# Performance work log

Hardware: AMD Instinct MI355X
Metric: run time of the kernel (lower is better)

## Reference

```python
import jax, jax.numpy as jnp
import numpy as np

# dims: B batch, T seq, DM d_model, H kv heads, D head dim
B, T, DM = 4, 2048, 768
H, D = 4, 64          # n_kv_heads, d_head = d_model // n_heads = 768 // 12
DIM = H * D           # 256


def setup_inputs() -> dict:
    key = jax.random.key(0)
    kx, kq, kk, kv, ko, kg = jax.random.split(key, 6)
    s = 0.02  # init scale for weights
    return {
        "x": jax.random.normal(kx, (B, T, DM), jnp.float32),
        "Wq": jax.random.normal(kq, (DM, DIM), jnp.float32) * s,
        "Wk": jax.random.normal(kk, (DM, DIM), jnp.float32) * s,
        "Wv": jax.random.normal(kv, (DM, DIM), jnp.float32) * s,
        "Wo": jax.random.normal(ko, (DIM, DM), jnp.float32) * s,
        "Wg": jax.random.normal(kg, (DM, DM), jnp.float32) * s,
    }


def _feature_map(x):
    # F.elu(x) + 1.0  (strictly positive features)
    return jax.nn.elu(x) + 1.0


def reference(x, Wq, Wk, Wv, Wo, Wg):
    Bx, Tx, _ = x.shape
    q = _feature_map((x @ Wq).reshape(Bx, Tx, H, D))
    k = _feature_map((x @ Wk).reshape(Bx, Tx, H, D))
    v = (x @ Wv).reshape(Bx, Tx, H, D)

    # time-major for scan: [T, B, H, D]
    qT = q.transpose(1, 0, 2, 3)
    kT = k.transpose(1, 0, 2, 3)
    vT = v.transpose(1, 0, 2, 3)

    S0 = jnp.zeros((Bx, H, D, D), x.dtype)  # running sum of k v^T
    z0 = jnp.zeros((Bx, H, D), x.dtype)     # running sum of k

    def step(carry, inp):
        S, z = carry
        qi, ki, vi = inp  # each [B, H, D]
        S = S + ki[..., :, None] * vi[..., None, :]   # outer product update
        z = z + ki
        num = jnp.einsum('bhd,bhde->bhe', qi, S)
        den = jnp.maximum(jnp.sum(qi * z, axis=-1), 1e-6)  # clamp(min=1e-6)
        return (S, z), num / den[..., None]

    (_, _), outT = jax.lax.scan(step, (S0, z0), (qT, kT, vT))

    out = outT.transpose(1, 0, 2, 3).reshape(Bx, Tx, DIM)  # [B, T, H*D]
    gate = jax.nn.sigmoid(x @ Wg)
    return (out @ Wo) * gate
```

## Files before the change

### kernel.cpp

```cpp
#include <hip/hip_runtime.h>
#include <math.h>

typedef __attribute__((ext_vector_type(8))) short bf16x8;
typedef __attribute__((ext_vector_type(4))) float f32x4;

namespace {
constexpr int Bb  = 4;
constexpr int Tt  = 2048;
constexpr int DM  = 768;
constexpr int Hh  = 4;
constexpr int Dd  = 64;
constexpr int DIM = 256;
constexpr int BT  = Bb * Tt;
constexpr int CH  = 64;
constexpr int NC  = Tt / CH;
constexpr int NQKVG = 1536;
constexpr int MT  = BT / 128;
}

__device__ __forceinline__ float elu1(float x) { return x > 0.f ? x + 1.f : expf(x); }

__device__ __forceinline__ unsigned short f2bf(float f) {
  unsigned int x = __float_as_uint(f);
  unsigned int r = (x + 0x7fffu + ((x >> 16) & 1u)) >> 16;
  return (unsigned short)r;
}
__device__ __forceinline__ float bf2f(unsigned short u) {
  return __uint_as_float((unsigned int)u << 16);
}

__device__ __forceinline__ void gload16(const void* g, void* l) {
  __builtin_amdgcn_global_load_lds(
      (const __attribute__((address_space(1))) void*)g,
      (__attribute__((address_space(3))) void*)l, 16, 0, 0);
}

struct Stage32 {
  const short* a[2];
  const short* b[2];
  int seg;
  __device__ __forceinline__ void init(const short* Ag, size_t lda,
                                       const short* Bg, size_t ldb, int w, int l) {
    const int c16 = (l & 3) ^ ((l >> 3) & 3);
    seg = w * 2;
#pragma unroll
    for (int j = 0; j < 2; ++j) {
      int row = (seg + j) * 16 + (l >> 2);
      a[j] = Ag + (size_t)row * lda + c16 * 8;
      b[j] = Bg + (size_t)row * ldb + c16 * 8;
    }
  }
  __device__ __forceinline__ void issue(int k0, short* as, short* bs) const {
#pragma unroll
    for (int j = 0; j < 2; ++j) {
      gload16(a[j] + k0, (char*)as + (seg + j) * 1024);
      gload16(b[j] + k0, (char*)bs + (seg + j) * 1024);
    }
  }
};

__device__ __forceinline__ void xcd_tile(int bid, int& mt, int& nt) {
  int xcd = bid & 7;
  int idx = bid >> 3;
  mt = xcd * 8 + (idx & 7);
  nt = idx >> 3;
}

__device__ __forceinline__ void read_frags(const short* as, const short* bs,
                                           bf16x8 (&af)[4], bf16x8 (&bf)[4],
                                           int wr, int wc, int lr, int lg) {
#pragma unroll
  for (int mi = 0; mi < 4; ++mi) {
    int r = wr * 64 + mi * 16 + lr;
    af[mi] = *(const bf16x8*)&as[r * 32 + (lg ^ ((r >> 1) & 3)) * 8];
  }
#pragma unroll
  for (int ni = 0; ni < 4; ++ni) {
    int r = wc * 64 + ni * 16 + lr;
    bf[ni] = *(const bf16x8*)&bs[r * 32 + (lg ^ ((r >> 1) & 3)) * 8];
  }
}

template <int NT>
__device__ __forceinline__ void kloop3p(const Stage32& st,
                                        short* A0, short* A1, short* A2,
                                        short* B0, short* B1, short* B2,
                                        f32x4 (&acc)[4][4], int wr, int wc,
                                        int lr, int lg) {
  st.issue(0, A0, B0);
  st.issue(32, A1, B1);
  asm volatile("s_waitcnt vmcnt(4)" ::: "memory");
  __builtin_amdgcn_s_barrier();
  bf16x8 af[4], bf[4];
  read_frags(A0, B0, af, bf, wr, wc, lr, lg);
  asm volatile("s_waitcnt lgkmcnt(0)" ::: "memory");
  __builtin_amdgcn_sched_barrier(0);
#pragma unroll
  for (int t = 0; t < NT; ++t) {
    if (t + 2 < NT) {
      short* an = (((t + 2) % 3) == 0) ? A0 : (((t + 2) % 3) == 1) ? A1 : A2;
      short* bn = (((t + 2) % 3) == 0) ? B0 : (((t + 2) % 3) == 1) ? B1 : B2;
      st.issue((t + 2) * 32, an, bn);
    }
    __builtin_amdgcn_s_setprio(1);
#pragma unroll
    for (int mi = 0; mi < 4; ++mi)
#pragma unroll
      for (int ni = 0; ni < 4; ++ni)
        acc[mi][ni] = __builtin_amdgcn_mfma_f32_16x16x32_bf16(
            af[mi], bf[ni], acc[mi][ni], 0, 0, 0);
    __builtin_amdgcn_s_setprio(0);
    if (t + 1 < NT) {
      if (t + 2 < NT)
        asm volatile("s_waitcnt vmcnt(4)" ::: "memory");
      else
        asm volatile("s_waitcnt vmcnt(0)" ::: "memory");
      __builtin_amdgcn_s_barrier();
      short* as = (((t + 1) % 3) == 0) ? A0 : (((t + 1) % 3) == 1) ? A1 : A2;
      short* bs = (((t + 1) % 3) == 0) ? B0 : (((t + 1) % 3) == 1) ? B1 : B2;
      read_frags(as, bs, af, bf, wr, wc, lr, lg);
      asm volatile("s_waitcnt lgkmcnt(0)" ::: "memory");
      __builtin_amdgcn_sched_barrier(0);
    }
  }
}

__global__ __launch_bounds__(256) void k_prep(
    const float* __restrict__ x, const float* __restrict__ Wq,
    const float* __restrict__ Wk, const float* __restrict__ Wv,
    const float* __restrict__ Wg, const float* __restrict__ Wo,
    unsigned short* __restrict__ xb, unsigned short* __restrict__ WT,
    unsigned short* __restrict__ WoT) {
  int bid = blockIdx.x;
  if (bid < 3072) {
    int i = bid * 256 + threadIdx.x;
    const float4* p = (const float4*)(x + (size_t)i * 8);
    float4 a = p[0], b = p[1];
    union { unsigned short u[8]; uint4 v; } r;
    r.u[0] = f2bf(a.x); r.u[1] = f2bf(a.y); r.u[2] = f2bf(a.z); r.u[3] = f2bf(a.w);
    r.u[4] = f2bf(b.x); r.u[5] = f2bf(b.y); r.u[6] = f2bf(b.z); r.u[7] = f2bf(b.w);
    *(uint4*)(xb + (size_t)i * 8) = r.v;
    return;
  }
  __shared__ float t[32][33];
  int idx = bid - 3072;
  const float* src;
  unsigned short* out;
  int K, N, n_off, ldo;
  if (idx < 576) {
    int z = idx / 192;
    idx %= 192;
    src = (z == 0) ? Wq : (z == 1) ? Wk : Wv;
    out = WT; K = 768; N = 256; n_off = z * 256; ldo = 768;
  } else if (idx < 1152) {
    idx -= 576;
    src = Wg; out = WT; K = 768; N = 768; n_off = 768; ldo = 768;
  } else {
    idx -= 1152;
    src = Wo; out = WoT; K = 256; N = 768; n_off = 0; ldo = 256;
  }
  int kt = idx % (K / 32), nt = idx / (K / 32);
  int k0 = kt * 32, n0 = nt * 32;
  const int tx = threadIdx.x & 31, ty = threadIdx.x >> 5;
  for (int i = ty; i < 32; i += 8)
    t[i][tx] = src[(size_t)(k0 + i) * N + n0 + tx];
  __syncthreads();
  for (int i = ty; i < 32; i += 8)
    out[(size_t)(n_off + n0 + i) * ldo + k0 + tx] = f2bf(t[tx][i]);
}

__global__ __launch_bounds__(256, 3) void k_gemm1(
    const unsigned short* __restrict__ xb, const unsigned short* __restrict__ WT,
    unsigned short* __restrict__ Q, unsigned short* __restrict__ K,
    unsigned short* __restrict__ V, unsigned short* __restrict__ G) {
  __shared__ __align__(16) char smem[49152];
  short* A0 = (short*)smem;
  short* A1 = (short*)(smem + 8192);
  short* A2 = (short*)(smem + 16384);
  short* B0 = (short*)(smem + 24576);
  short* B1 = (short*)(smem + 32768);
  short* B2 = (short*)(smem + 40960);
  const int tid = threadIdx.x;
  const int w = tid >> 6, l = tid & 63;
  const int lr = l & 15, lg = l >> 4;
  const int wr = w >> 1, wc = w & 1;
  int mt, nt;
  xcd_tile(blockIdx.x, mt, nt);
  const int m0 = mt * 128, n0 = nt * 128;

  Stage32 st;
  st.init((const short*)xb + (size_t)m0 * DM, DM,
          (const short*)WT + (size_t)n0 * DM, DM, w, l);

  f32x4 acc[4][4];
#pragma unroll
  for (int i = 0; i < 4; ++i)
#pragma unroll
    for (int j = 0; j < 4; ++j) acc[i][j] = (f32x4){0.f, 0.f, 0.f, 0.f};

  kloop3p<DM / 32>(st, A0, A1, A2, B0, B1, B2, acc, wr, wc, lr, lg);
  __syncthreads();

  const int ttype = (n0 < 512) ? 0 : (n0 < 768) ? 1 : 2;
  unsigned short* Cs = (unsigned short*)smem;
#pragma unroll
  for (int mi = 0; mi < 4; ++mi)
#pragma unroll
    for (int ni = 0; ni < 4; ++ni)
#pragma unroll
      for (int r = 0; r < 4; ++r) {
        float v = acc[mi][ni][r];
        if (ttype == 0) v = elu1(v);
        else if (ttype == 2) v = 1.f / (1.f + expf(-v));
        Cs[(wr * 64 + mi * 16 + lg * 4 + r) * 128 + wc * 64 + ni * 16 + lr] =
            f2bf(v);
      }
  __syncthreads();
  unsigned short* dst;
  int ldd, cb;
  if (n0 < 256)      { dst = Q; ldd = DIM; cb = n0; }
  else if (n0 < 512) { dst = K; ldd = DIM; cb = n0 - 256; }
  else if (n0 < 768) { dst = V; ldd = DIM; cb = n0 - 512; }
  else               { dst = G; ldd = DM;  cb = n0 - 768; }
  const uint4* Cv = (const uint4*)Cs;
#pragma unroll
  for (int i = 0; i < 8; ++i) {
    int idx = tid + i * 256;
    int urow = idx >> 4, uc = idx & 15;
    *(uint4*)(dst + (size_t)(m0 + urow) * ldd + cb + uc * 8) = Cv[idx];
  }
}

__global__ __launch_bounds__(256) void k_chunksum(
    const unsigned short* __restrict__ K, const unsigned short* __restrict__ V,
    unsigned short* __restrict__ Sc, float* __restrict__ zc) {
  __shared__ __align__(16) char smem[16384];
  short* Kt = (short*)smem;
  short* Vt = (short*)(smem + 8192);
  const int c = blockIdx.x, h = blockIdx.y, b = blockIdx.z;
  const int tid = threadIdx.x;
  const int w = tid >> 6, l = tid & 63;
  const int lr = l & 15, lg = l >> 4;
  const size_t rowbase = ((size_t)(b * Tt + c * CH)) * DIM + h * Dd;

#pragma unroll
  for (int it = 0; it < 4; ++it) {
    int idx = tid + it * 256;
    int t = idx >> 4, d4 = idx & 15;
    short4 k4 = *(const short4*)((const short*)K + rowbase + (size_t)t * DIM + d4 * 4);
    short4 v4 = *(const short4*)((const short*)V + rowbase + (size_t)t * DIM + d4 * 4);
    const short* kk = (const short*)&k4;
    const short* vv = (const short*)&v4;
#pragma unroll
    for (int j = 0; j < 4; ++j) {
      int e = d4 * 4 + j;
      int sl = ((t >> 3) ^ (e & 7)) * 16 + (t & 7) * 2;
      *(short*)((char*)Kt + e * 128 + sl) = kk[j];
      *(short*)((char*)Vt + e * 128 + sl) = vv[j];
    }
  }
  __syncthreads();

  if (tid < Dd) {
    float s = 0.f;
    for (int t = 0; t < CH; ++t) {
      unsigned short u = *(const unsigned short*)(
          (char*)Kt + tid * 128 + (((t >> 3) ^ (tid & 7)) * 16) + (t & 7) * 2);
      s += bf2f(u);
    }
    zc[((size_t)(b * Hh + h) * NC + c) * Dd + tid] = s;
  }

  f32x4 a[4];
#pragma unroll
  for (int nf = 0; nf < 4; ++nf) a[nf] = (f32x4){0.f, 0.f, 0.f, 0.f};
  const int rd = w * 16 + lr;
#pragma unroll
  for (int ks = 0; ks < 2; ++ks) {
    bf16x8 af = *(const bf16x8*)((char*)Kt + rd * 128 +
                                 (((ks * 4 + lg) ^ (rd & 7)) * 16));
#pragma unroll
    for (int nf = 0; nf < 4; ++nf) {
      int re = nf * 16 + lr;
      bf16x8 bf = *(const bf16x8*)((char*)Vt + re * 128 +
                                   (((ks * 4 + lg) ^ (re & 7)) * 16));
      a[nf] = __builtin_amdgcn_mfma_f32_16x16x32_bf16(af, bf, a[nf], 0, 0, 0);
    }
  }
  __syncthreads();

  unsigned short* Cb = (unsigned short*)smem;
#pragma unroll
  for (int nf = 0; nf < 4; ++nf)
#pragma unroll
    for (int r = 0; r < 4; ++r)
      Cb[(w * 16 + lg * 4 + r) * 64 + nf * 16 + lr] = f2bf(a[nf][r]);
  __syncthreads();
  const size_t base = ((size_t)(b * Hh + h) * NC + c) * (Dd * Dd);
  const uint4* Cv = (const uint4*)Cb;
#pragma unroll
  for (int it = 0; it < 2; ++it) {
    int idx = tid + it * 256;
    *(uint4*)&Sc[base + (size_t)idx * 8] = Cv[idx];
  }
}

__global__ __launch_bounds__(256) void k_scan(unsigned short* __restrict__ Sc,
                                              float* __restrict__ zc) {
  const int bh = blockIdx.x;
  const int o = blockIdx.y * 256 + threadIdx.x;
  const size_t base = (size_t)bh * NC * (Dd * Dd) + o;
  float run = 0.f;
#pragma unroll
  for (int c = 0; c < NC; ++c) {
    size_t off = base + (size_t)c * (Dd * Dd);
    float cur = bf2f(Sc[off]);
    Sc[off] = f2bf(run);
    run += cur;
  }
  if (blockIdx.y == 0 && threadIdx.x < Dd) {
    float rz = 0.f;
    for (int c = 0; c < NC; ++c) {
      size_t oz = ((size_t)bh * NC + c) * Dd + threadIdx.x;
      float cur = zc[oz];
      zc[oz] = rz;
      rz += cur;
    }
  }
}

__global__ __launch_bounds__(256) void k_out(
    const unsigned short* __restrict__ Q, const unsigned short* __restrict__ K,
    const unsigned short* __restrict__ V, const unsigned short* __restrict__ Sc,
    const float* __restrict__ zc, unsigned short* __restrict__ O) {
  __shared__ __align__(16) char smem[41216];
  short* Qs = (short*)smem;
  short* Ks = (short*)(smem + 8192);
  short* Vt = (short*)(smem + 16384);
  short* St = (short*)(smem + 24576);
  short* Ps = (short*)(smem + 32768);
  float* zs = (float*)(smem + 40960);
  const int c = blockIdx.x, h = blockIdx.y, b = blockIdx.z;
  const int tid = threadIdx.x;
  const int w = tid >> 6, l = tid & 63;
  const int lr = l & 15, lg = l >> 4;
  const size_t rowbase = ((size_t)(b * Tt + c * CH)) * DIM + h * Dd;

  {
    const int c16 = (l & 7) ^ ((l >> 3) & 7);
#pragma unroll
    for (int i = 0; i < 2; ++i) {
      int row = i * 32 + w * 8 + (l >> 3);
      gload16((const short*)Q + rowbase + (size_t)row * DIM + c16 * 8,
              (char*)Qs + (i * 32 + w * 8) * 128);
      gload16((const short*)K + rowbase + (size_t)row * DIM + c16 * 8,
              (char*)Ks + (i * 32 + w * 8) * 128);
    }
  }
  const size_t sbase = ((size_t)(b * Hh + h) * NC + c) * (Dd * Dd);
  if (tid < Dd) zs[tid] = zc[((size_t)(b * Hh + h) * NC + c) * Dd + tid];
#pragma unroll
  for (int it = 0; it < 4; ++it) {
    int idx = tid + it * 256;
    int t = idx >> 4, d4 = idx & 15;
    short4 v4 = *(const short4*)((const short*)V + rowbase + (size_t)t * DIM + d4 * 4);
    const short* vv = (const short*)&v4;
#pragma unroll
    for (int j = 0; j < 4; ++j) {
      int e = d4 * 4 + j;
      *(short*)((char*)Vt + e * 128 + (((t >> 3) ^ (e & 7)) * 16) + (t & 7) * 2) = vv[j];
    }
    short4 s4 = *(const short4*)((const short*)Sc + sbase + (size_t)t * 64 + d4 * 4);
    const short* sv = (const short*)&s4;
#pragma unroll
    for (int j = 0; j < 4; ++j) {
      int e = d4 * 4 + j;
      *(short*)((char*)St + e * 128 + (((t >> 3) ^ (e & 7)) * 16) + (t & 7) * 2) =
          sv[j];
    }
  }
  __syncthreads();

  f32x4 a0[4];
#pragma unroll
  for (int nf = 0; nf < 4; ++nf) a0[nf] = (f32x4){0.f, 0.f, 0.f, 0.f};
  const int rq = w * 16 + lr;
#pragma unroll
  for (int ks = 0; ks < 2; ++ks) {
    bf16x8 af = *(const bf16x8*)((char*)Qs + rq * 128 +
                                 (((ks * 4 + lg) ^ (rq & 7)) * 16));
#pragma unroll
    for (int nf = 0; nf < 4; ++nf) {
      int rk = nf * 16 + lr;
      bf16x8 bf = *(const bf16x8*)((char*)Ks + rk * 128 +
                                   (((ks * 4 + lg) ^ (rk & 7)) * 16));
      a0[nf] = __builtin_amdgcn_mfma_f32_16x16x32_bf16(af, bf, a0[nf], 0, 0, 0);
    }
  }

  float part[4] = {0.f, 0.f, 0.f, 0.f};
#pragma unroll
  for (int nf = 0; nf < 4; ++nf) {
    int col = nf * 16 + lr;
#pragma unroll
    for (int r = 0; r < 4; ++r) {
      int row = w * 16 + lg * 4 + r;
      float av = (col <= row) ? a0[nf][r] : 0.f;
      part[r] += av;
      *(short*)((char*)Ps + row * 128 +
                ((((nf * 2) + (lr >> 3)) ^ (row & 7)) * 16) + (lr & 7) * 2) =
          (short)f2bf(av);
    }
  }
#pragma unroll
  for (int r = 0; r < 4; ++r) {
    int row = w * 16 + lg * 4 + r;
#pragma unroll
    for (int j = 0; j < 4; ++j) {
      int d = lr + j * 16;
      unsigned short qu = *(const unsigned short*)(
          (char*)Qs + row * 128 + (((d >> 3) ^ (row & 7)) * 16) + (d & 7) * 2);
      part[r] += bf2f(qu) * zs[d];
    }
  }
  float inv[4];
#pragma unroll
  for (int r = 0; r < 4; ++r) {
    float s = part[r];
    s += __shfl_xor(s, 1);
    s += __shfl_xor(s, 2);
    s += __shfl_xor(s, 4);
    s += __shfl_xor(s, 8);
    inv[r] = 1.f / fmaxf(s, 1e-6f);
  }
  __syncthreads();

  f32x4 a1[4];
#pragma unroll
  for (int nf = 0; nf < 4; ++nf) a1[nf] = (f32x4){0.f, 0.f, 0.f, 0.f};
#pragma unroll
  for (int ks = 0; ks < 4; ++ks) {
    const char* abase = (ks < 2) ? (const char*)Ps : (const char*)Qs;
    const char* bbase = (ks < 2) ? (const char*)Vt : (const char*)St;
    int kslot = (ks & 1) * 4 + lg;
    bf16x8 af = *(const bf16x8*)(abase + rq * 128 + ((kslot ^ (rq & 7)) * 16));
#pragma unroll
    for (int nf = 0; nf < 4; ++nf) {
      int re = nf * 16 + lr;
      bf16x8 bf = *(const bf16x8*)(bbase + re * 128 + ((kslot ^ (re & 7)) * 16));
      a1[nf] = __builtin_amdgcn_mfma_f32_16x16x32_bf16(af, bf, a1[nf], 0, 0, 0);
    }
  }
  __syncthreads();

#pragma unroll
  for (int nf = 0; nf < 4; ++nf)
#pragma unroll
    for (int r = 0; r < 4; ++r) {
      int row = w * 16 + lg * 4 + r;
      Ps[row * 64 + nf * 16 + lr] = (short)f2bf(a1[nf][r] * inv[r]);
    }
  __syncthreads();
  const uint4* Pv = (const uint4*)Ps;
#pragma unroll
  for (int i = 0; i < 2; ++i) {
    int idx = tid + i * 256;
    int row = idx >> 3, uc = idx & 7;
    *(uint4*)((unsigned short*)O + rowbase + (size_t)row * DIM + uc * 8) = Pv[idx];
  }
}

__global__ __launch_bounds__(256, 3) void k_gemm2(
    const unsigned short* __restrict__ Ob, const unsigned short* __restrict__ WoT,
    const unsigned short* __restrict__ G, float* __restrict__ out) {
  __shared__ __align__(16) char smem[49152];
  short* A0 = (short*)smem;
  short* A1 = (short*)(smem + 8192);
  short* A2 = (short*)(smem + 16384);
  short* B0 = (short*)(smem + 24576);
  short* B1 = (short*)(smem + 32768);
  short* B2 = (short*)(smem + 40960);
  const int tid = threadIdx.x;
  const int w = tid >> 6, l = tid & 63;
  const int lr = l & 15, lg = l >> 4;
  const int wr = w >> 1, wc = w & 1;
  int mt, nt;
  xcd_tile(blockIdx.x, mt, nt);
  const int m0 = mt * 128, n0 = nt * 128;

  Stage32 st;
  st.init((const short*)Ob + (size_t)m0 * DIM, DIM,
          (const short*)WoT + (size_t)n0 * DIM, DIM, w, l);

  f32x4 acc[4][4];
#pragma unroll
  for (int i = 0; i < 4; ++i)
#pragma unroll
    for (int j = 0; j < 4; ++j) acc[i][j] = (f32x4){0.f, 0.f, 0.f, 0.f};

  kloop3p<DIM / 32>(st, A0, A1, A2, B0, B1, B2, acc, wr, wc, lr, lg);

  float* Cf = (float*)smem;
#pragma unroll
  for (int half = 0; half < 2; ++half) {
    __syncthreads();
    if (wr == half) {
#pragma unroll
      for (int mi = 0; mi < 4; ++mi)
#pragma unroll
        for (int ni = 0; ni < 4; ++ni)
#pragma unroll
          for (int r = 0; r < 4; ++r)
            Cf[(mi * 16 + lg * 4 + r) * 128 + wc * 64 + ni * 16 + lr] =
                acc[mi][ni][r];
    }
    __syncthreads();
    const float4* Cv = (const float4*)Cf;
#pragma unroll
    for (int i = 0; i < 8; ++i) {
      int idx = tid + i * 256;
      int urow = idx >> 5, uc = idx & 31;
      float4 cv = Cv[idx];
      size_t go = (size_t)(m0 + half * 64 + urow) * DM + n0 + uc * 4;
      short4 g4 = *(const short4*)(G + go);
      float4 ov;
      ov.x = cv.x * bf2f(g4.x);
      ov.y = cv.y * bf2f(g4.y);
      ov.z = cv.z * bf2f(g4.z);
      ov.w = cv.w * bf2f(g4.w);
      *(float4*)(out + go) = ov;
    }
  }
}

extern "C" void kernel_launch(void* const* d_in, const int* in_sizes, int n_in,
                              void* d_out, int out_size, void* d_ws,
                              size_t ws_size, hipStream_t stream) {
  const float* x  = (const float*)d_in[0];
  const float* Wq = (const float*)d_in[1];
  const float* Wk = (const float*)d_in[2];
  const float* Wv = (const float*)d_in[3];
  const float* Wo = (const float*)d_in[4];
  const float* Wg = (const float*)d_in[5];
  float* out = (float*)d_out;

  char* p = (char*)d_ws;
  size_t off = 0;
  auto alloc = [&](size_t bytes) {
    void* r = p + off;
    off = (off + bytes + 255) & ~(size_t)255;
    return r;
  };
  unsigned short* xb  = (unsigned short*)alloc((size_t)BT * DM * 2);
  unsigned short* WT  = (unsigned short*)alloc((size_t)NQKVG * DM * 2);
  unsigned short* WoT = (unsigned short*)alloc((size_t)DM * DIM * 2);
  unsigned short* Q   = (unsigned short*)alloc((size_t)BT * DIM * 2);
  unsigned short* Kf  = (unsigned short*)alloc((size_t)BT * DIM * 2);
  unsigned short* Vf  = (unsigned short*)alloc((size_t)BT * DIM * 2);
  unsigned short* G   = (unsigned short*)alloc((size_t)BT * DM * 2);
  unsigned short* Ob  = (unsigned short*)alloc((size_t)BT * DIM * 2);
  unsigned short* Sc  = (unsigned short*)alloc((size_t)Bb * Hh * NC * Dd * Dd * 2);
  float* zc = (float*)alloc((size_t)Bb * Hh * NC * Dd * 4);

  k_prep<<<dim3(3072 + 1344), dim3(256), 0, stream>>>(x, Wq, Wk, Wv, Wg, Wo,
                                                      xb, WT, WoT);

  k_gemm1<<<dim3(MT * (NQKVG / 128)), dim3(256), 0, stream>>>(
      xb, WT, Q, Kf, Vf, G);

  k_chunksum<<<dim3(NC, Hh, Bb), dim3(256), 0, stream>>>(Kf, Vf, Sc, zc);
  k_scan<<<dim3(Bb * Hh, Dd * Dd / 256), dim3(256), 0, stream>>>(Sc, zc);
  k_out<<<dim3(NC, Hh, Bb), dim3(256), 0, stream>>>(Q, Kf, Vf, Sc, zc, Ob);

  k_gemm2<<<dim3(MT * (DM / 128)), dim3(256), 0, stream>>>(Ob, WoT, G, out);
}
```

Measured before the change: 74.25 us.

## Fold chunk-state prefix scan into output kernel, dropping separate scan launch

Removes the k_scan kernel. Each k_out block now sums the per-chunk KV states and z vectors of all preceding chunks itself, instead of reading a precomputed exclusive prefix. This drops one kernel launch and the serial read-modify-write pass over Sc. In exchange the redundant reads grow quadratically with chunk count (up to 31 chunk states per block), which makes the work per block uneven. Accumulation now runs in fp32 across chunks and is rounded to bf16 once, rather than the running sum being rounded at each chunk.

```diff
diff --git a/kernel.cpp b/kernel.cpp
--- a/kernel.cpp
+++ b/kernel.cpp
@@ -305,30 +305,6 @@
   }
 }
 
-__global__ __launch_bounds__(256) void k_scan(unsigned short* __restrict__ Sc,
-                                              float* __restrict__ zc) {
-  const int bh = blockIdx.x;
-  const int o = blockIdx.y * 256 + threadIdx.x;
-  const size_t base = (size_t)bh * NC * (Dd * Dd) + o;
-  float run = 0.f;
-#pragma unroll
-  for (int c = 0; c < NC; ++c) {
-    size_t off = base + (size_t)c * (Dd * Dd);
-    float cur = bf2f(Sc[off]);
-    Sc[off] = f2bf(run);
-    run += cur;
-  }
-  if (blockIdx.y == 0 && threadIdx.x < Dd) {
-    float rz = 0.f;
-    for (int c = 0; c < NC; ++c) {
-      size_t oz = ((size_t)bh * NC + c) * Dd + threadIdx.x;
-      float cur = zc[oz];
-      zc[oz] = rz;
-      rz += cur;
-    }
-  }
-}
-
 __global__ __launch_bounds__(256) void k_out(
     const unsigned short* __restrict__ Q, const unsigned short* __restrict__ K,
     const unsigned short* __restrict__ V, const unsigned short* __restrict__ Sc,
@@ -357,8 +333,13 @@
               (char*)Ks + (i * 32 + w * 8) * 128);
     }
   }
-  const size_t sbase = ((size_t)(b * Hh + h) * NC + c) * (Dd * Dd);
-  if (tid < Dd) zs[tid] = zc[((size_t)(b * Hh + h) * NC + c) * Dd + tid];
+  const size_t bh = (size_t)(b * Hh + h);
+  if (tid < Dd) {
+    float rz = 0.f;
+    for (int cp = 0; cp < c; ++cp)
+      rz += zc[(bh * NC + cp) * Dd + tid];
+    zs[tid] = rz;
+  }
 #pragma unroll
   for (int it = 0; it < 4; ++it) {
     int idx = tid + it * 256;
@@ -370,20 +351,28 @@
       int e = d4 * 4 + j;
       *(short*)((char*)Vt + e * 128 + (((t >> 3) ^ (e & 7)) * 16) + (t & 7) * 2) = vv[j];
     }
-    short4 s4 = *(const short4*)((const short*)Sc + sbase + (size_t)t * 64 + d4 * 4);
-    const short* sv = (const short*)&s4;
+    float a0 = 0.f, a1 = 0.f, a2 = 0.f, a3 = 0.f;
+    const unsigned short* sp = Sc + bh * NC * (Dd * Dd) + (size_t)t * 64 + d4 * 4;
+    for (int cp = 0; cp < c; ++cp) {
+      short4 s4 = *(const short4*)(sp + (size_t)cp * (Dd * Dd));
+      a0 += bf2f((unsigned short)s4.x);
+      a1 += bf2f((unsigned short)s4.y);
+      a2 += bf2f((unsigned short)s4.z);
+      a3 += bf2f((unsigned short)s4.w);
+    }
+    float av[4] = {a0, a1, a2, a3};
 #pragma unroll
     for (int j = 0; j < 4; ++j) {
       int e = d4 * 4 + j;
       *(short*)((char*)St + e * 128 + (((t >> 3) ^ (e & 7)) * 16) + (t & 7) * 2) =
-          sv[j];
-    }
-  }
-  __syncthreads();
-
-  f32x4 a0[4];
-#pragma unroll
-  for (int nf = 0; nf < 4; ++nf) a0[nf] = (f32x4){0.f, 0.f, 0.f, 0.f};
+          (short)f2bf(av[j]);
+    }
+  }
+  __syncthreads();
+
+  f32x4 a0q[4];
+#pragma unroll
+  for (int nf = 0; nf < 4; ++nf) a0q[nf] = (f32x4){0.f, 0.f, 0.f, 0.f};
   const int rq = w * 16 + lr;
 #pragma unroll
   for (int ks = 0; ks < 2; ++ks) {
@@ -394,7 +383,7 @@
       int rk = nf * 16 + lr;
       bf16x8 bf = *(const bf16x8*)((char*)Ks + rk * 128 +
                                    (((ks * 4 + lg) ^ (rk & 7)) * 16));
-      a0[nf] = __builtin_amdgcn_mfma_f32_16x16x32_bf16(af, bf, a0[nf], 0, 0, 0);
+      a0q[nf] = __builtin_amdgcn_mfma_f32_16x16x32_bf16(af, bf, a0q[nf], 0, 0, 0);
     }
   }
 
@@ -405,7 +394,7 @@
 #pragma unroll
     for (int r = 0; r < 4; ++r) {
       int row = w * 16 + lg * 4 + r;
-      float av = (col <= row) ? a0[nf][r] : 0.f;
+      float av = (col <= row) ? a0q[nf][r] : 0.f;
       part[r] += av;
       *(short*)((char*)Ps + row * 128 +
                 ((((nf * 2) + (lr >> 3)) ^ (row & 7)) * 16) + (lr & 7) * 2) =
@@ -435,9 +424,9 @@
   }
   __syncthreads();
 
-  f32x4 a1[4];
-#pragma unroll
-  for (int nf = 0; nf < 4; ++nf) a1[nf] = (f32x4){0.f, 0.f, 0.f, 0.f};
+  f32x4 a1q[4];
+#pragma unroll
+  for (int nf = 0; nf < 4; ++nf) a1q[nf] = (f32x4){0.f, 0.f, 0.f, 0.f};
 #pragma unroll
   for (int ks = 0; ks < 4; ++ks) {
     const char* abase = (ks < 2) ? (const char*)Ps : (const char*)Qs;
@@ -448,7 +437,7 @@
     for (int nf = 0; nf < 4; ++nf) {
       int re = nf * 16 + lr;
       bf16x8 bf = *(const bf16x8*)(bbase + re * 128 + ((kslot ^ (re & 7)) * 16));
-      a1[nf] = __builtin_amdgcn_mfma_f32_16x16x32_bf16(af, bf, a1[nf], 0, 0, 0);
+      a1q[nf] = __builtin_amdgcn_mfma_f32_16x16x32_bf16(af, bf, a1q[nf], 0, 0, 0);
     }
   }
   __syncthreads();
@@ -458,7 +447,7 @@
 #pragma unroll
     for (int r = 0; r < 4; ++r) {
       int row = w * 16 + lg * 4 + r;
-      Ps[row * 64 + nf * 16 + lr] = (short)f2bf(a1[nf][r] * inv[r]);
+      Ps[row * 64 + nf * 16 + lr] = (short)f2bf(a1q[nf][r] * inv[r]);
     }
   __syncthreads();
   const uint4* Pv = (const uint4*)Ps;
@@ -569,7 +558,6 @@
       xb, WT, Q, Kf, Vf, G);
 
   k_chunksum<<<dim3(NC, Hh, Bb), dim3(256), 0, stream>>>(Kf, Vf, Sc, zc);
-  k_scan<<<dim3(Bb * Hh, Dd * Dd / 256), dim3(256), 0, stream>>>(Sc, zc);
   k_out<<<dim3(NC, Hh, Bb), dim3(256), 0, stream>>>(Q, Kf, Vf, Sc, zc, Ob);
 
   k_gemm2<<<dim3(MT * (DM / 128)), dim3(256), 0, stream>>>(Ob, WoT, G, out);
```

New measurement: 99.01 us. 33.3% more time.

## Fuse chunk prefix scan into chunksum via last-block atomic counter

Applied to the files above, without the earlier changes.

Removes the separate k_scan launch. The last block to finish per (batch, head), detected with an atomic counter that k_prep resets, runs the exclusive prefix scan over the chunk states. Each of its threads handles 16 contiguous elements with vectorized loads, so only 16 blocks do the serial scan while the rest exit. This saves one launch and its gap, at the cost of serializing the scan onto fewer blocks (16 instead of 256) and relying on threadfence/atomic ordering.

```diff
diff --git a/kernel.cpp b/kernel.cpp
--- a/kernel.cpp
+++ b/kernel.cpp
@@ -130,9 +130,10 @@
     const float* __restrict__ Wk, const float* __restrict__ Wv,
     const float* __restrict__ Wg, const float* __restrict__ Wo,
     unsigned short* __restrict__ xb, unsigned short* __restrict__ WT,
-    unsigned short* __restrict__ WoT) {
+    unsigned short* __restrict__ WoT, int* __restrict__ cnt) {
   int bid = blockIdx.x;
   if (bid < 3072) {
+    if (bid == 0 && threadIdx.x < 16) cnt[threadIdx.x] = 0;
     int i = bid * 256 + threadIdx.x;
     const float4* p = (const float4*)(x + (size_t)i * 8);
     float4 a = p[0], b = p[1];
@@ -233,8 +234,10 @@
 
 __global__ __launch_bounds__(256) void k_chunksum(
     const unsigned short* __restrict__ K, const unsigned short* __restrict__ V,
-    unsigned short* __restrict__ Sc, float* __restrict__ zc) {
+    unsigned short* __restrict__ Sc, float* __restrict__ zc,
+    int* __restrict__ cnt) {
   __shared__ __align__(16) char smem[16384];
+  __shared__ int s_last;
   short* Kt = (short*)smem;
   short* Vt = (short*)(smem + 8192);
   const int c = blockIdx.x, h = blockIdx.y, b = blockIdx.z;
@@ -296,35 +299,60 @@
     for (int r = 0; r < 4; ++r)
       Cb[(w * 16 + lg * 4 + r) * 64 + nf * 16 + lr] = f2bf(a[nf][r]);
   __syncthreads();
-  const size_t base = ((size_t)(b * Hh + h) * NC + c) * (Dd * Dd);
+  const int bh = b * Hh + h;
+  const size_t base = ((size_t)bh * NC + c) * (Dd * Dd);
   const uint4* Cv = (const uint4*)Cb;
 #pragma unroll
   for (int it = 0; it < 2; ++it) {
     int idx = tid + it * 256;
     *(uint4*)&Sc[base + (size_t)idx * 8] = Cv[idx];
   }
-}
-
-__global__ __launch_bounds__(256) void k_scan(unsigned short* __restrict__ Sc,
-                                              float* __restrict__ zc) {
-  const int bh = blockIdx.x;
-  const int o = blockIdx.y * 256 + threadIdx.x;
-  const size_t base = (size_t)bh * NC * (Dd * Dd) + o;
-  float run = 0.f;
-#pragma unroll
-  for (int c = 0; c < NC; ++c) {
-    size_t off = base + (size_t)c * (Dd * Dd);
-    float cur = bf2f(Sc[off]);
-    Sc[off] = f2bf(run);
-    run += cur;
-  }
-  if (blockIdx.y == 0 && threadIdx.x < Dd) {
+
+  __threadfence();
+  __syncthreads();
+  if (tid == 0) {
+    int old = atomicAdd(&cnt[bh], 1);
+    s_last = (old == NC - 1) ? 1 : 0;
+  }
+  __syncthreads();
+  if (!s_last) return;
+  __threadfence();
+
+  const size_t bhbase = (size_t)bh * NC * (Dd * Dd);
+  float run[16];
+#pragma unroll
+  for (int s = 0; s < 16; ++s) run[s] = 0.f;
+  for (int c2 = 0; c2 < NC; ++c2) {
+    unsigned short* p = Sc + bhbase + (size_t)c2 * (Dd * Dd) + (size_t)tid * 16;
+    uint4 v0 = *(uint4*)p;
+    uint4 v1 = *(uint4*)(p + 8);
+    unsigned short* e0 = (unsigned short*)&v0;
+    unsigned short* e1 = (unsigned short*)&v1;
+#pragma unroll
+    for (int s = 0; s < 8; ++s) {
+      float cur = bf2f(e0[s]);
+      e0[s] = f2bf(run[s]);
+      run[s] += cur;
+    }
+#pragma unroll
+    for (int s = 0; s < 8; ++s) {
+      float cur = bf2f(e1[s]);
+      e1[s] = f2bf(run[8 + s]);
+      run[8 + s] += cur;
+    }
+    *(uint4*)p = v0;
+    *(uint4*)(p + 8) = v1;
+  }
+  if (tid < Dd) {
+    float vals[NC];
+#pragma unroll
+    for (int c2 = 0; c2 < NC; ++c2)
+      vals[c2] = zc[((size_t)bh * NC + c2) * Dd + tid];
     float rz = 0.f;
-    for (int c = 0; c < NC; ++c) {
-      size_t oz = ((size_t)bh * NC + c) * Dd + threadIdx.x;
-      float cur = zc[oz];
-      zc[oz] = rz;
-      rz += cur;
+#pragma unroll
+    for (int c2 = 0; c2 < NC; ++c2) {
+      zc[((size_t)bh * NC + c2) * Dd + tid] = rz;
+      rz += vals[c2];
     }
   }
 }
@@ -561,15 +589,15 @@
   unsigned short* Ob  = (unsigned short*)alloc((size_t)BT * DIM * 2);
   unsigned short* Sc  = (unsigned short*)alloc((size_t)Bb * Hh * NC * Dd * Dd * 2);
   float* zc = (float*)alloc((size_t)Bb * Hh * NC * Dd * 4);
+  int* cnt  = (int*)alloc(16 * sizeof(int));
 
   k_prep<<<dim3(3072 + 1344), dim3(256), 0, stream>>>(x, Wq, Wk, Wv, Wg, Wo,
-                                                      xb, WT, WoT);
+                                                      xb, WT, WoT, cnt);
 
   k_gemm1<<<dim3(MT * (NQKVG / 128)), dim3(256), 0, stream>>>(
       xb, WT, Q, Kf, Vf, G);
 
-  k_chunksum<<<dim3(NC, Hh, Bb), dim3(256), 0, stream>>>(Kf, Vf, Sc, zc);
-  k_scan<<<dim3(Bb * Hh, Dd * Dd / 256), dim3(256), 0, stream>>>(Sc, zc);
+  k_chunksum<<<dim3(NC, Hh, Bb), dim3(256), 0, stream>>>(Kf, Vf, Sc, zc, cnt);
   k_out<<<dim3(NC, Hh, Bb), dim3(256), 0, stream>>>(Q, Kf, Vf, Sc, zc, Ob);
 
   k_gemm2<<<dim3(MT * (DM / 128)), dim3(256), 0, stream>>>(Ob, WoT, G, out);
```

Result: slower. 139.0 us (+87.2%).

## Fuse fp32-to-bf16 conversion of x into the QKVG GEMM A-tile load

Applied to the files above, without the earlier changes.

Removes the separate pass that converts x to a bf16 buffer. The first GEMM now loads fp32 x directly into registers, converts it and writes swizzled bf16 into LDS, pipelined alongside the async B-tile loads. This saves one write and one read of the bf16 copy of x, and makes k_prep smaller. In exchange, each of the 12 N-tile blocks re-reads fp32 x, which is twice the bytes of bf16. The conversion ALU work and extra VGPRs now sit in the GEMM loop, which may reduce overlap or occupancy.

```diff
diff --git a/kernel.cpp b/kernel.cpp
--- a/kernel.cpp
+++ b/kernel.cpp
@@ -125,25 +125,31 @@
   }
 }
 
+__device__ __forceinline__ void loadA(const float* ag, int k0, float4 (&v)[4]) {
+#pragma unroll
+  for (int i = 0; i < 4; ++i) v[i] = *(const float4*)(ag + k0 + i * 4);
+}
+
+__device__ __forceinline__ void cvtwriteA(short* Abuf, int arow, int ah, int axk,
+                                          const float4 (&v)[4]) {
+  union { unsigned short u[8]; uint4 q; } p0, p1;
+  const float* f = (const float*)&v[0];
+#pragma unroll
+  for (int i = 0; i < 8; ++i) p0.u[i] = f2bf(f[i]);
+#pragma unroll
+  for (int i = 0; i < 8; ++i) p1.u[i] = f2bf(f[8 + i]);
+  char* base = (char*)Abuf + arow * 64;
+  *(uint4*)(base + (((2 * ah + 0) ^ axk) * 16)) = p0.q;
+  *(uint4*)(base + (((2 * ah + 1) ^ axk) * 16)) = p1.q;
+}
+
 __global__ __launch_bounds__(256) void k_prep(
-    const float* __restrict__ x, const float* __restrict__ Wq,
-    const float* __restrict__ Wk, const float* __restrict__ Wv,
-    const float* __restrict__ Wg, const float* __restrict__ Wo,
-    unsigned short* __restrict__ xb, unsigned short* __restrict__ WT,
+    const float* __restrict__ Wq, const float* __restrict__ Wk,
+    const float* __restrict__ Wv, const float* __restrict__ Wg,
+    const float* __restrict__ Wo, unsigned short* __restrict__ WT,
     unsigned short* __restrict__ WoT) {
-  int bid = blockIdx.x;
-  if (bid < 3072) {
-    int i = bid * 256 + threadIdx.x;
-    const float4* p = (const float4*)(x + (size_t)i * 8);
-    float4 a = p[0], b = p[1];
-    union { unsigned short u[8]; uint4 v; } r;
-    r.u[0] = f2bf(a.x); r.u[1] = f2bf(a.y); r.u[2] = f2bf(a.z); r.u[3] = f2bf(a.w);
-    r.u[4] = f2bf(b.x); r.u[5] = f2bf(b.y); r.u[6] = f2bf(b.z); r.u[7] = f2bf(b.w);
-    *(uint4*)(xb + (size_t)i * 8) = r.v;
-    return;
-  }
   __shared__ float t[32][33];
-  int idx = bid - 3072;
+  int idx = blockIdx.x;
   const float* src;
   unsigned short* out;
   int K, N, n_off, ldo;
@@ -170,7 +176,7 @@
 }
 
 __global__ __launch_bounds__(256, 3) void k_gemm1(
-    const unsigned short* __restrict__ xb, const unsigned short* __restrict__ WT,
+    const float* __restrict__ x, const unsigned short* __restrict__ WT,
     unsigned short* __restrict__ Q, unsigned short* __restrict__ K,
     unsigned short* __restrict__ V, unsigned short* __restrict__ G) {
   __shared__ __align__(16) char smem[49152];
@@ -188,9 +194,15 @@
   xcd_tile(blockIdx.x, mt, nt);
   const int m0 = mt * 128, n0 = nt * 128;
 
-  Stage32 st;
-  st.init((const short*)xb + (size_t)m0 * DM, DM,
-          (const short*)WT + (size_t)n0 * DM, DM, w, l);
+  const int c16 = (l & 3) ^ ((l >> 3) & 3);
+  const int bseg = w * 2;
+  const short* bg0 = (const short*)WT +
+                     (size_t)(n0 + bseg * 16 + (l >> 2)) * DM + c16 * 8;
+  const short* bg1 = (const short*)WT +
+                     (size_t)(n0 + (bseg + 1) * 16 + (l >> 2)) * DM + c16 * 8;
+  const int arow = tid >> 1, ah = tid & 1;
+  const int axk = (arow >> 1) & 3;
+  const float* ag = x + (size_t)(m0 + arow) * DM + ah * 16;
 
   f32x4 acc[4][4];
 #pragma unroll
@@ -198,7 +210,53 @@
 #pragma unroll
     for (int j = 0; j < 4; ++j) acc[i][j] = (f32x4){0.f, 0.f, 0.f, 0.f};
 
-  kloop3p<DM / 32>(st, A0, A1, A2, B0, B1, B2, acc, wr, wc, lr, lg);
+  constexpr int NT = DM / 32;
+  float4 va0[4], va1[4];
+  bf16x8 af[4], bf[4];
+
+  gload16(bg0, (char*)B0 + bseg * 1024);
+  gload16(bg1, (char*)B0 + (bseg + 1) * 1024);
+  loadA(ag, 0, va0);
+  gload16(bg0 + 32, (char*)B1 + bseg * 1024);
+  gload16(bg1 + 32, (char*)B1 + (bseg + 1) * 1024);
+  loadA(ag, 32, va1);
+  cvtwriteA(A0, arow, ah, axk, va0);
+  asm volatile("s_waitcnt lgkmcnt(0)" ::: "memory");
+  __builtin_amdgcn_s_barrier();
+  read_frags(A0, B0, af, bf, wr, wc, lr, lg);
+  asm volatile("s_waitcnt lgkmcnt(0)" ::: "memory");
+  __builtin_amdgcn_sched_barrier(0);
+
+#pragma unroll
+  for (int t = 0; t < NT; ++t) {
+    if (t + 2 < NT) {
+      short* bn = (((t + 2) % 3) == 0) ? B0 : (((t + 2) % 3) == 1) ? B1 : B2;
+      gload16(bg0 + (t + 2) * 32, (char*)bn + bseg * 1024);
+      gload16(bg1 + (t + 2) * 32, (char*)bn + (bseg + 1) * 1024);
+      if ((t & 1) == 0) loadA(ag, (t + 2) * 32, va0);
+      else              loadA(ag, (t + 2) * 32, va1);
+    }
+    __builtin_amdgcn_s_setprio(1);
+#pragma unroll
+    for (int mi = 0; mi < 4; ++mi)
+#pragma unroll
+      for (int ni = 0; ni < 4; ++ni)
+        acc[mi][ni] = __builtin_amdgcn_mfma_f32_16x16x32_bf16(
+            af[mi], bf[ni], acc[mi][ni], 0, 0, 0);
+    __builtin_amdgcn_s_setprio(0);
+    __builtin_amdgcn_sched_barrier(0);
+    if (t + 1 < NT) {
+      short* an = (((t + 1) % 3) == 0) ? A0 : (((t + 1) % 3) == 1) ? A1 : A2;
+      short* bn = (((t + 1) % 3) == 0) ? B0 : (((t + 1) % 3) == 1) ? B1 : B2;
+      if (((t + 1) & 1) == 0) cvtwriteA(an, arow, ah, axk, va0);
+      else                    cvtwriteA(an, arow, ah, axk, va1);
+      asm volatile("s_waitcnt lgkmcnt(0)" ::: "memory");
+      __builtin_amdgcn_s_barrier();
+      read_frags(an, bn, af, bf, wr, wc, lr, lg);
+      asm volatile("s_waitcnt lgkmcnt(0)" ::: "memory");
+      __builtin_amdgcn_sched_barrier(0);
+    }
+  }
   __syncthreads();
 
   const int ttype = (n0 < 512) ? 0 : (n0 < 768) ? 1 : 2;
@@ -551,7 +609,6 @@
     off = (off + bytes + 255) & ~(size_t)255;
     return r;
   };
-  unsigned short* xb  = (unsigned short*)alloc((size_t)BT * DM * 2);
   unsigned short* WT  = (unsigned short*)alloc((size_t)NQKVG * DM * 2);
   unsigned short* WoT = (unsigned short*)alloc((size_t)DM * DIM * 2);
   unsigned short* Q   = (unsigned short*)alloc((size_t)BT * DIM * 2);
@@ -562,11 +619,10 @@
   unsigned short* Sc  = (unsigned short*)alloc((size_t)Bb * Hh * NC * Dd * Dd * 2);
   float* zc = (float*)alloc((size_t)Bb * Hh * NC * Dd * 4);
 
-  k_prep<<<dim3(3072 + 1344), dim3(256), 0, stream>>>(x, Wq, Wk, Wv, Wg, Wo,
-                                                      xb, WT, WoT);
+  k_prep<<<dim3(1344), dim3(256), 0, stream>>>(Wq, Wk, Wv, Wg, Wo, WT, WoT);
 
   k_gemm1<<<dim3(MT * (NQKVG / 128)), dim3(256), 0, stream>>>(
-      xb, WT, Q, Kf, Vf, G);
+      x, WT, Q, Kf, Vf, G);
 
   k_chunksum<<<dim3(NC, Hh, Bb), dim3(256), 0, stream>>>(Kf, Vf, Sc, zc);
   k_scan<<<dim3(Bb * Hh, Dd * Dd / 256), dim3(256), 0, stream>>>(Sc, zc);
```

Measured after the change: 80.05 us. 7.8% more time.
